# Kernel optimization log

Measured on AMD Instinct MI355X. Metric: run time of the kernel, lower is better.

The kernel has to match this reference:

```python
import jax, jax.numpy as jnp
import numpy as np

B, L, D = 32, 2048, 1024


def setup_inputs() -> dict:
    key = jax.random.key(0)
    ks = jax.random.split(key, 8)
    s = 1.0 / np.sqrt(D).astype(np.float32)  # torch nn.Linear init scale
    return {
        "decoder_hidden": jax.random.normal(ks[0], (B, 1, D), jnp.float32),
        "encoder_outputs": jax.random.normal(ks[1], (B, L, D), jnp.float32),
        "W_w": jax.random.uniform(ks[2], (D, D), jnp.float32, -s, s),
        "W_b": jax.random.uniform(ks[3], (D,), jnp.float32, -s, s),
        "U_w": jax.random.uniform(ks[4], (D, D), jnp.float32, -s, s),
        "U_b": jax.random.uniform(ks[5], (D,), jnp.float32, -s, s),
        "v_w": jax.random.uniform(ks[6], (1, D), jnp.float32, -s, s),
        "v_b": jax.random.uniform(ks[7], (1,), jnp.float32, -s, s),
    }


def reference(decoder_hidden, encoder_outputs, W_w, W_b, U_w, U_b, v_w, v_b):
    # torch Linear: y = x @ W.T + b
    q = decoder_hidden @ W_w.T + W_b            # [B, 1, D]
    k = encoder_outputs @ U_w.T + U_b           # [B, L, D]
    scores = jnp.tanh(q + k) @ v_w.T + v_b      # [B, L, 1]
    attn = jax.nn.softmax(scores[..., 0], axis=-1)[:, None, :]  # [B, 1, L]
    context = jnp.einsum("bql,bld->bqd", attn, encoder_outputs)  # [B, 1, D]
    return (context, attn)
```

## Files before the change

kernel.cpp:

```cpp
#include <hip/hip_runtime.h>
#include <hip/hip_bf16.h>

#define BB 32
#define LL 2048
#define DD 1024

typedef short short8 __attribute__((ext_vector_type(8)));
typedef float f32x4  __attribute__((ext_vector_type(4)));

__device__ __forceinline__ short f2bf(float f) {
    unsigned u = __float_as_uint(f);
    u += 0x7fffu + ((u >> 16) & 1u);
    return (short)(u >> 16);
}

__device__ __forceinline__ float fast_tanh(float x) {
    float e = __expf(2.f * x);
    return 1.f - 2.f * __builtin_amdgcn_rcpf(e + 1.f);
}

__global__ void cvt_u_kernel(const float* __restrict__ U, short* __restrict__ Ubf) {
    int idx = (blockIdx.x * 256 + threadIdx.x) * 8;
    float4 a = *(const float4*)(U + idx);
    float4 c = *(const float4*)(U + idx + 4);
    short8 p;
    p[0] = f2bf(a.x); p[1] = f2bf(a.y); p[2] = f2bf(a.z); p[3] = f2bf(a.w);
    p[4] = f2bf(c.x); p[5] = f2bf(c.y); p[6] = f2bf(c.z); p[7] = f2bf(c.w);
    *(short8*)(Ubf + idx) = p;
}

__global__ void q_kernel(const float* __restrict__ dh, const float* __restrict__ Ww,
                         const float* __restrict__ Wb, const float* __restrict__ Ub,
                         float* __restrict__ qbuf) {
    int b  = blockIdx.x >> 4;
    int d0 = (blockIdx.x & 15) << 6;
    int t = threadIdx.x, w = t >> 6, lane = t & 63;
    __shared__ __align__(16) float hs[DD];
    *(float4*)&hs[t * 4] = *(const float4*)&dh[b * DD + t * 4];
    __syncthreads();
    float hr[16];
#pragma unroll
    for (int i = 0; i < 16; i++) hr[i] = hs[lane + 64 * i];
    for (int i = 0; i < 16; i++) {
        int d = d0 + w * 16 + i;
        const float* wr = Ww + (size_t)d * DD;
        float s = 0.f;
#pragma unroll
        for (int j = 0; j < 16; j++) s += wr[lane + 64 * j] * hr[j];
#pragma unroll
        for (int m = 1; m < 64; m <<= 1) s += __shfl_xor(s, m, 64);
        if (lane == 0) qbuf[b * DD + d] = s + Wb[d] + Ub[d];
    }
}

__global__ __launch_bounds__(256, 3) void gemm_scores_kernel(
    const float* __restrict__ enc, const short* __restrict__ Ubf,
    const float* __restrict__ qbuf, const float* __restrict__ vw,
    float* __restrict__ scores) {
    __shared__ __align__(16) short As[128 * 32];
    __shared__ __align__(16) short Bs[128 * 32];
    __shared__ float q_s[128], v_s[128], s_acc[128];

    const int t = threadIdx.x;
    const int lane = t & 63, w = t >> 6;
    const int l15 = lane & 15, quad = lane >> 4;
    const int wm = w >> 1, wn = w & 1;
    const int n0 = blockIdx.x << 7;
    const int m0 = blockIdx.y << 7;
    const int b  = m0 >> 11;

    if (t < 128) {
        q_s[t] = qbuf[(b << 10) + n0 + t];
        v_s[t] = vw[n0 + t];
        s_acc[t] = 0.f;
    }

    f32x4 acc[4][4];
#pragma unroll
    for (int i = 0; i < 4; i++)
#pragma unroll
        for (int j = 0; j < 4; j++) acc[i][j] = (f32x4){0.f, 0.f, 0.f, 0.f};

    const int arow = t >> 1, ahalf = t & 1;
    const float* aptr = enc + (((size_t)(m0 + arow)) << 10) + (ahalf << 4);
    short* adst = As + arow * 32 + ahalf * 16;
    const int brow = t >> 2, bks = (t & 3) * 8;
    const short* bptr1 = Ubf + ((size_t)(n0 + brow)) * 1024 + bks;
    const short* bptr2 = bptr1 + (size_t)64 * 1024;
    short* bdst1 = Bs + brow * 32 + bks;
    short* bdst2 = bdst1 + 64 * 32;

    for (int k0 = 0; k0 < 1024; k0 += 32) {
        __syncthreads();
        float4 f0 = *(const float4*)(aptr + k0);
        float4 f1 = *(const float4*)(aptr + k0 + 4);
        float4 f2 = *(const float4*)(aptr + k0 + 8);
        float4 f3 = *(const float4*)(aptr + k0 + 12);
        short8 p0, p1;
        p0[0] = f2bf(f0.x); p0[1] = f2bf(f0.y); p0[2] = f2bf(f0.z); p0[3] = f2bf(f0.w);
        p0[4] = f2bf(f1.x); p0[5] = f2bf(f1.y); p0[6] = f2bf(f1.z); p0[7] = f2bf(f1.w);
        p1[0] = f2bf(f2.x); p1[1] = f2bf(f2.y); p1[2] = f2bf(f2.z); p1[3] = f2bf(f2.w);
        p1[4] = f2bf(f3.x); p1[5] = f2bf(f3.y); p1[6] = f2bf(f3.z); p1[7] = f2bf(f3.w);
        *(short8*)adst = p0;
        *(short8*)(adst + 8) = p1;
        *(short8*)bdst1 = *(const short8*)(bptr1 + k0);
        *(short8*)bdst2 = *(const short8*)(bptr2 + k0);
        __syncthreads();

        short8 af[4], bfv[4];
#pragma unroll
        for (int mt = 0; mt < 4; mt++)
            af[mt] = *(const short8*)&As[(wm * 64 + mt * 16 + l15) * 32 + quad * 8];
#pragma unroll
        for (int nt = 0; nt < 4; nt++)
            bfv[nt] = *(const short8*)&Bs[(wn * 64 + nt * 16 + l15) * 32 + quad * 8];
#pragma unroll
        for (int mt = 0; mt < 4; mt++)
#pragma unroll
            for (int nt = 0; nt < 4; nt++)
                acc[mt][nt] = __builtin_amdgcn_mfma_f32_16x16x32_bf16(
                    af[mt], bfv[nt], acc[mt][nt], 0, 0, 0);
    }

    float qn[4], vn[4];
#pragma unroll
    for (int nt = 0; nt < 4; nt++) {
        qn[nt] = q_s[wn * 64 + nt * 16 + l15];
        vn[nt] = v_s[wn * 64 + nt * 16 + l15];
    }
#pragma unroll
    for (int mt = 0; mt < 4; mt++) {
#pragma unroll
        for (int r = 0; r < 4; r++) {
            float sum = 0.f;
#pragma unroll
            for (int nt = 0; nt < 4; nt++) {
                float x = acc[mt][nt][r] + qn[nt];
                sum += vn[nt] * fast_tanh(x);
            }
            sum += __shfl_xor(sum, 1, 64);
            sum += __shfl_xor(sum, 2, 64);
            sum += __shfl_xor(sum, 4, 64);
            sum += __shfl_xor(sum, 8, 64);
            if (l15 == 0)
                atomicAdd(&s_acc[wm * 64 + mt * 16 + quad * 4 + r], sum);
        }
    }
    __syncthreads();
    if (t < 128) atomicAdd(&scores[m0 + t], s_acc[t]);
}

__global__ void softmax_kernel(const float* __restrict__ scores, float* __restrict__ attn) {
    int b = blockIdx.x, t = threadIdx.x;
    int w = t >> 6, lane = t & 63;
    __shared__ float rm[4], rs[4];
    float v[8];
#pragma unroll
    for (int i = 0; i < 8; i++) v[i] = scores[(b << 11) + t + (i << 8)];
    float m = v[0];
#pragma unroll
    for (int i = 1; i < 8; i++) m = fmaxf(m, v[i]);
#pragma unroll
    for (int s = 1; s < 64; s <<= 1) m = fmaxf(m, __shfl_xor(m, s, 64));
    if (lane == 0) rm[w] = m;
    __syncthreads();
    m = fmaxf(fmaxf(rm[0], rm[1]), fmaxf(rm[2], rm[3]));
    float s = 0.f;
#pragma unroll
    for (int i = 0; i < 8; i++) { v[i] = __expf(v[i] - m); s += v[i]; }
#pragma unroll
    for (int k = 1; k < 64; k <<= 1) s += __shfl_xor(s, k, 64);
    if (lane == 0) rs[w] = s;
    __syncthreads();
    s = rs[0] + rs[1] + rs[2] + rs[3];
    float inv = 1.f / s;
#pragma unroll
    for (int i = 0; i < 8; i++) attn[(b << 11) + t + (i << 8)] = v[i] * inv;
}

__global__ void context_kernel(const float* __restrict__ enc, const float* __restrict__ attn,
                               float* __restrict__ ctx) {
    int dchunk = blockIdx.x, lsp = blockIdx.y, b = blockIdx.z;
    int t = threadIdx.x;
    int d4 = (t & 31) << 2;
    int dl = t >> 5;
    int lbase = lsp << 9;
    __shared__ __align__(16) float at_s[512];
    at_s[t] = attn[(b << 11) + lbase + t];
    at_s[t + 256] = attn[(b << 11) + lbase + t + 256];
    __syncthreads();
    int d0 = dchunk << 7;
    float ax = 0.f, ay = 0.f, az = 0.f, aw = 0.f;
    const float* base = enc + (((size_t)(b << 11) + lbase) << 10) + d0 + d4;
#pragma unroll 4
    for (int i = 0; i < 64; i++) {
        int l = (i << 3) + dl;
        float wgt = at_s[l];
        float4 e = *(const float4*)(base + ((size_t)l << 10));
        ax += wgt * e.x; ay += wgt * e.y; az += wgt * e.z; aw += wgt * e.w;
    }
    float* o = ctx + (b << 10) + d0 + d4;
    atomicAdd(o + 0, ax);
    atomicAdd(o + 1, ay);
    atomicAdd(o + 2, az);
    atomicAdd(o + 3, aw);
}

extern "C" void kernel_launch(void* const* d_in, const int* in_sizes, int n_in,
                              void* d_out, int out_size, void* d_ws, size_t ws_size,
                              hipStream_t stream) {
    const float* dh  = (const float*)d_in[0];
    const float* enc = (const float*)d_in[1];
    const float* Ww  = (const float*)d_in[2];
    const float* Wb  = (const float*)d_in[3];
    const float* Uw  = (const float*)d_in[4];
    const float* Ub  = (const float*)d_in[5];
    const float* vw  = (const float*)d_in[6];

    float* out  = (float*)d_out;
    char*  ws   = (char*)d_ws;
    short* Ubf    = (short*)ws;
    float* qbuf   = (float*)(ws + (1 << 21));
    float* scores = (float*)(ws + (1 << 21) + (1 << 17));

    hipMemsetAsync(scores, 0, (size_t)BB * LL * sizeof(float), stream);
    hipMemsetAsync(out, 0, (size_t)BB * DD * sizeof(float), stream);

    cvt_u_kernel<<<512, 256, 0, stream>>>(Uw, Ubf);
    q_kernel<<<512, 256, 0, stream>>>(dh, Ww, Wb, Ub, qbuf);
    gemm_scores_kernel<<<dim3(8, 512), 256, 0, stream>>>(enc, Ubf, qbuf, vw, scores);
    softmax_kernel<<<BB, 256, 0, stream>>>(scores, out + BB * DD);
    context_kernel<<<dim3(8, 4, BB), 256, 0, stream>>>(enc, out + BB * DD, out);
}
```

Measured before the change: 657.0 us.

## Pre-convert encoder outputs to bf16 and stream GEMM tiles via direct-to-LDS loads

When the workspace is large enough, the encoder outputs are converted to bf16 once in a separate pass. The scores GEMM then loads bf16 tiles straight into LDS with global_load_lds, so the fp32-to-bf16 conversion no longer sits inside the inner loop and each of the 8 column blocks re-reads half as many bytes. Per-column-block partial scores are written to separate buffers and summed in the softmax kernel, which removes the atomics and the memset. The context kernel now covers the full sequence per block and reduces through shared memory instead of global atomics. The cost is an extra 128MB bf16 write plus its re-read, and a dependency on the workspace size.

```diff
diff --git a/kernel.cpp b/kernel.cpp
--- a/kernel.cpp
+++ b/kernel.cpp
@@ -1,5 +1,6 @@
 #include <hip/hip_runtime.h>
 #include <hip/hip_bf16.h>
+#include <stdint.h>
 
 #define BB 32
 #define LL 2048
@@ -19,14 +20,20 @@
     return 1.f - 2.f * __builtin_amdgcn_rcpf(e + 1.f);
 }
 
-__global__ void cvt_u_kernel(const float* __restrict__ U, short* __restrict__ Ubf) {
+__device__ __forceinline__ void async_cp16(const void* g, void* l) {
+    __builtin_amdgcn_global_load_lds(
+        (__attribute__((address_space(1))) void*)g,
+        (__attribute__((address_space(3))) void*)l, 16, 0, 0);
+}
+
+__global__ void cvt_bf16_kernel(const float* __restrict__ src, short* __restrict__ dst) {
     int idx = (blockIdx.x * 256 + threadIdx.x) * 8;
-    float4 a = *(const float4*)(U + idx);
-    float4 c = *(const float4*)(U + idx + 4);
+    float4 a = *(const float4*)(src + idx);
+    float4 c = *(const float4*)(src + idx + 4);
     short8 p;
     p[0] = f2bf(a.x); p[1] = f2bf(a.y); p[2] = f2bf(a.z); p[3] = f2bf(a.w);
     p[4] = f2bf(c.x); p[5] = f2bf(c.y); p[6] = f2bf(c.z); p[7] = f2bf(c.w);
-    *(short8*)(Ubf + idx) = p;
+    *(short8*)(dst + idx) = p;
 }
 
 __global__ void q_kernel(const float* __restrict__ dh, const float* __restrict__ Ww,
@@ -53,7 +60,90 @@
     }
 }
 
-__global__ __launch_bounds__(256, 3) void gemm_scores_kernel(
+__global__ __launch_bounds__(256, 3) void gemm_scores_bf(
+    const short* __restrict__ encbf, const short* __restrict__ Ubf,
+    const float* __restrict__ qbuf, const float* __restrict__ vw,
+    float* __restrict__ spart) {
+    __shared__ __align__(16) short As[128 * 32];
+    __shared__ __align__(16) short Bs[128 * 32];
+    __shared__ float q_s[128], v_s[128], s_acc[2][128];
+
+    const int t = threadIdx.x;
+    const int lane = t & 63, w = t >> 6;
+    const int l15 = lane & 15, quad = lane >> 4;
+    const int wm = w >> 1, wn = w & 1;
+    const int n0 = blockIdx.x << 7;
+    const int m0 = blockIdx.y << 7;
+    const int b  = m0 >> 11;
+
+    if (t < 128) {
+        q_s[t] = qbuf[(b << 10) + n0 + t];
+        v_s[t] = vw[n0 + t];
+    }
+
+    f32x4 acc[4][4];
+#pragma unroll
+    for (int i = 0; i < 4; i++)
+#pragma unroll
+        for (int j = 0; j < 4; j++) acc[i][j] = (f32x4){0.f, 0.f, 0.f, 0.f};
+
+    const int srow = lane >> 2, sseg = (lane & 3) << 3;
+    const short* gA0 = encbf + (((size_t)(m0 + w * 32 + srow)) << 10) + sseg;
+    const short* gB0 = Ubf   + (((size_t)(n0 + w * 32 + srow)) << 10) + sseg;
+    short* lA0 = As + w * 32 * 32;
+    short* lB0 = Bs + w * 32 * 32;
+
+    for (int k0 = 0; k0 < 1024; k0 += 32) {
+        __syncthreads();
+        async_cp16(gA0 + k0, lA0);
+        async_cp16(gA0 + k0 + (16 << 10), lA0 + 16 * 32);
+        async_cp16(gB0 + k0, lB0);
+        async_cp16(gB0 + k0 + (16 << 10), lB0 + 16 * 32);
+        __syncthreads();
+
+        short8 af[4], bfv[4];
+#pragma unroll
+        for (int mt = 0; mt < 4; mt++)
+            af[mt] = *(const short8*)&As[(wm * 64 + mt * 16 + l15) * 32 + quad * 8];
+#pragma unroll
+        for (int nt = 0; nt < 4; nt++)
+            bfv[nt] = *(const short8*)&Bs[(wn * 64 + nt * 16 + l15) * 32 + quad * 8];
+#pragma unroll
+        for (int mt = 0; mt < 4; mt++)
+#pragma unroll
+            for (int nt = 0; nt < 4; nt++)
+                acc[mt][nt] = __builtin_amdgcn_mfma_f32_16x16x32_bf16(
+                    af[mt], bfv[nt], acc[mt][nt], 0, 0, 0);
+    }
+
+    float qn[4], vn[4];
+#pragma unroll
+    for (int nt = 0; nt < 4; nt++) {
+        qn[nt] = q_s[wn * 64 + nt * 16 + l15];
+        vn[nt] = v_s[wn * 64 + nt * 16 + l15];
+    }
+#pragma unroll
+    for (int mt = 0; mt < 4; mt++) {
+#pragma unroll
+        for (int r = 0; r < 4; r++) {
+            float sum = 0.f;
+#pragma unroll
+            for (int nt = 0; nt < 4; nt++)
+                sum += vn[nt] * fast_tanh(acc[mt][nt][r] + qn[nt]);
+            sum += __shfl_xor(sum, 1, 64);
+            sum += __shfl_xor(sum, 2, 64);
+            sum += __shfl_xor(sum, 4, 64);
+            sum += __shfl_xor(sum, 8, 64);
+            if (l15 == 0)
+                s_acc[wn][wm * 64 + mt * 16 + quad * 4 + r] = sum;
+        }
+    }
+    __syncthreads();
+    if (t < 128)
+        spart[((size_t)blockIdx.x << 16) + m0 + t] = s_acc[0][t] + s_acc[1][t];
+}
+
+__global__ __launch_bounds__(256, 3) void gemm_scores_f32(
     const float* __restrict__ enc, const short* __restrict__ Ubf,
     const float* __restrict__ qbuf, const float* __restrict__ vw,
     float* __restrict__ scores) {
@@ -134,10 +224,8 @@
         for (int r = 0; r < 4; r++) {
             float sum = 0.f;
 #pragma unroll
-            for (int nt = 0; nt < 4; nt++) {
-                float x = acc[mt][nt][r] + qn[nt];
-                sum += vn[nt] * fast_tanh(x);
-            }
+            for (int nt = 0; nt < 4; nt++)
+                sum += vn[nt] * fast_tanh(acc[mt][nt][r] + qn[nt]);
             sum += __shfl_xor(sum, 1, 64);
             sum += __shfl_xor(sum, 2, 64);
             sum += __shfl_xor(sum, 4, 64);
@@ -150,13 +238,18 @@
     if (t < 128) atomicAdd(&scores[m0 + t], s_acc[t]);
 }
 
-__global__ void softmax_kernel(const float* __restrict__ scores, float* __restrict__ attn) {
+__global__ void softmax_kernel(const float* __restrict__ sp, int npart,
+                               float* __restrict__ attn) {
     int b = blockIdx.x, t = threadIdx.x;
     int w = t >> 6, lane = t & 63;
     __shared__ float rm[4], rs[4];
     float v[8];
 #pragma unroll
-    for (int i = 0; i < 8; i++) v[i] = scores[(b << 11) + t + (i << 8)];
+    for (int i = 0; i < 8; i++) {
+        float s = 0.f;
+        for (int p = 0; p < npart; p++) s += sp[p * 65536 + (b << 11) + t + (i << 8)];
+        v[i] = s;
+    }
     float m = v[0];
 #pragma unroll
     for (int i = 1; i < 8; i++) m = fmaxf(m, v[i]);
@@ -180,30 +273,35 @@
 
 __global__ void context_kernel(const float* __restrict__ enc, const float* __restrict__ attn,
                                float* __restrict__ ctx) {
-    int dchunk = blockIdx.x, lsp = blockIdx.y, b = blockIdx.z;
+    int dchunk = blockIdx.x, b = blockIdx.y;
     int t = threadIdx.x;
+    __shared__ __align__(16) float at_s[2048];
+    __shared__ float red[16][128];
+    *(float4*)&at_s[t * 4] = *(const float4*)&attn[(b << 11) + t * 4];
+    __syncthreads();
     int d4 = (t & 31) << 2;
     int dl = t >> 5;
-    int lbase = lsp << 9;
-    __shared__ __align__(16) float at_s[512];
-    at_s[t] = attn[(b << 11) + lbase + t];
-    at_s[t + 256] = attn[(b << 11) + lbase + t + 256];
-    __syncthreads();
     int d0 = dchunk << 7;
+    const float* base = enc + ((size_t)b << 21) + d0 + d4;
     float ax = 0.f, ay = 0.f, az = 0.f, aw = 0.f;
-    const float* base = enc + (((size_t)(b << 11) + lbase) << 10) + d0 + d4;
 #pragma unroll 4
-    for (int i = 0; i < 64; i++) {
-        int l = (i << 3) + dl;
-        float wgt = at_s[l];
+    for (int i = 0; i < 128; i++) {
+        int l = (i << 4) + dl;
+        float wg = at_s[l];
         float4 e = *(const float4*)(base + ((size_t)l << 10));
-        ax += wgt * e.x; ay += wgt * e.y; az += wgt * e.z; aw += wgt * e.w;
-    }
-    float* o = ctx + (b << 10) + d0 + d4;
-    atomicAdd(o + 0, ax);
-    atomicAdd(o + 1, ay);
-    atomicAdd(o + 2, az);
-    atomicAdd(o + 3, aw);
+        ax += wg * e.x; ay += wg * e.y; az += wg * e.z; aw += wg * e.w;
+    }
+    red[dl][d4 + 0] = ax;
+    red[dl][d4 + 1] = ay;
+    red[dl][d4 + 2] = az;
+    red[dl][d4 + 3] = aw;
+    __syncthreads();
+    if (t < 128) {
+        float s = 0.f;
+#pragma unroll
+        for (int j = 0; j < 16; j++) s += red[j][t];
+        ctx[(b << 10) + d0 + t] = s;
+    }
 }
 
 extern "C" void kernel_launch(void* const* d_in, const int* in_sizes, int n_in,
@@ -218,17 +316,26 @@
     const float* vw  = (const float*)d_in[6];
 
     float* out  = (float*)d_out;
+    float* attn = out + BB * DD;
     char*  ws   = (char*)d_ws;
-    short* Ubf    = (short*)ws;
-    float* qbuf   = (float*)(ws + (1 << 21));
-    float* scores = (float*)(ws + (1 << 21) + (1 << 17));
-
-    hipMemsetAsync(scores, 0, (size_t)BB * LL * sizeof(float), stream);
-    hipMemsetAsync(out, 0, (size_t)BB * DD * sizeof(float), stream);
-
-    cvt_u_kernel<<<512, 256, 0, stream>>>(Uw, Ubf);
+    short* Ubf   = (short*)ws;
+    float* qbuf  = (float*)(ws + (2 << 20));
+    float* sbuf  = (float*)(ws + (2 << 20) + (1 << 17));
+    short* encbf = (short*)(ws + (8 << 20));
+
+    bool bigws = ws_size >= ((size_t)143 << 20);
+
+    cvt_bf16_kernel<<<512, 256, 0, stream>>>(Uw, Ubf);
     q_kernel<<<512, 256, 0, stream>>>(dh, Ww, Wb, Ub, qbuf);
-    gemm_scores_kernel<<<dim3(8, 512), 256, 0, stream>>>(enc, Ubf, qbuf, vw, scores);
-    softmax_kernel<<<BB, 256, 0, stream>>>(scores, out + BB * DD);
-    context_kernel<<<dim3(8, 4, BB), 256, 0, stream>>>(enc, out + BB * DD, out);
-}
+
+    if (bigws) {
+        cvt_bf16_kernel<<<32768, 256, 0, stream>>>(enc, encbf);
+        gemm_scores_bf<<<dim3(8, 512), 256, 0, stream>>>(encbf, Ubf, qbuf, vw, sbuf);
+        softmax_kernel<<<BB, 256, 0, stream>>>(sbuf, 8, attn);
+    } else {
+        hipMemsetAsync(sbuf, 0, (size_t)BB * LL * sizeof(float), stream);
+        gemm_scores_f32<<<dim3(8, 512), 256, 0, stream>>>(enc, Ubf, qbuf, vw, sbuf);
+        softmax_kernel<<<BB, 256, 0, stream>>>(sbuf, 1, attn);
+    }
+    context_kernel<<<dim3(8, BB), 512, 0, stream>>>(enc, attn, out);
+}
```

Result: faster. 637.7 us (-2.9%).
